# Performance work log

Hardware: AMD Instinct MI355X
Metric: run time of the kernel (lower is better)

The kernel has to match this reference:

```python
import jax, jax.numpy as jnp
import numpy as np
from jax import lax

B, CI, CO, H, W = 8, 128, 256, 56, 56
P, K = 9, 3  # num_paths, kernel_size


def setup_inputs() -> dict:
    key = jax.random.key(0)
    ks = jax.random.split(key, 7)
    s_conv = 1.0 / np.sqrt(CI * K * K)
    s_o1 = 1.0 / np.sqrt(CI)
    s_o2 = 1.0 / np.sqrt(CO // 2)
    return {
        "x": jax.random.normal(ks[0], (B, CI, H, W), dtype=jnp.float32),
        # num_paths independent 3x3 convs, stacked on leading axis
        "kw": jax.random.uniform(ks[1], (P, CO, CI, K, K), jnp.float32, -s_conv, s_conv),
        "kb": jax.random.uniform(ks[2], (P, CO), jnp.float32, -s_conv, s_conv),
        # observer: 1x1 conv CI -> CO//2, tanh, 1x1 conv CO//2 -> P
        "ow1": jax.random.uniform(ks[3], (CO // 2, CI), jnp.float32, -s_o1, s_o1),
        "ob1": jax.random.uniform(ks[4], (CO // 2,), jnp.float32, -s_o1, s_o1),
        "ow2": jax.random.uniform(ks[5], (P, CO // 2), jnp.float32, -s_o2, s_o2),
        "ob2": jax.random.uniform(ks[6], (P,), jnp.float32, -s_o2, s_o2),
    }


def reference(x, kw, kb, ow1, ob1, ow2, ob2):
    p, co, ci, k, _ = kw.shape
    b, _, h, w = x.shape
    # All num_paths convs as a single grouped-output conv: (P*CO, CI, K, K)
    wflat = kw.reshape(p * co, ci, k, k)
    paths = lax.conv_general_dilated(
        x, wflat, window_strides=(1, 1), padding=((1, 1), (1, 1)),
        dimension_numbers=("NCHW", "OIHW", "NCHW"))
    paths = paths + kb.reshape(p * co)[None, :, None, None]
    paths = paths.reshape(b, p, co, h, w)  # [B,P,CO,H,W]

    # observer: two 1x1 convs (pure channel mixes) with tanh in between
    hmid = jnp.tanh(jnp.einsum("bchw,dc->bdhw", x, ow1) + ob1[None, :, None, None])
    scores = jnp.einsum("bdhw,pd->bphw", hmid, ow2) + ob2[None, :, None, None]

    # eval-mode collapse: argmax over paths, pixel-wise hard selection.
    # (one-hot multiply + sum over paths == gather of the winning path)
    idx = jnp.argmax(scores, axis=1)  # [B,H,W]
    out = jnp.take_along_axis(paths, idx[:, None, None, :, :], axis=1)[:, 0]  # [B,CO,H,W]
    return jax.nn.relu(out)  # norm_type='none' -> identity norm
```

## Files before the change

kernel.cpp:

```cpp
#include <hip/hip_runtime.h>
#include <hip/hip_bf16.h>


typedef unsigned int u32;

#define NPIX    25088
#define OFF_LIST 4096
#define OFF_XPAD 907264
#define OFF_W2   7796736
#define OFF_P2R  13105152
#define OFF_OUTC 13205504

__device__ __forceinline__ unsigned short f2bf(float f) {
  u32 u = __builtin_bit_cast(u32, f);
  u32 r = (u + 0x7FFFu + ((u >> 16) & 1u)) >> 16;
  return (unsigned short)r;
}
__device__ __forceinline__ float bflo(u32 w) {
  return __builtin_bit_cast(float, w << 16);
}
__device__ __forceinline__ float bfhi(u32 w) {
  return __builtin_bit_cast(float, w & 0xFFFF0000u);
}

#define GLDS16(g, l)                                                        \
  __builtin_amdgcn_global_load_lds(                                         \
      (const __attribute__((address_space(1))) u32*)(g),                    \
      (__attribute__((address_space(3))) u32*)(l), 16, 0, 0)
#define GLDS4(g, l)                                                         \
  __builtin_amdgcn_global_load_lds(                                         \
      (const __attribute__((address_space(1))) u32*)(g),                    \
      (__attribute__((address_space(3))) u32*)(l), 4, 0, 0)

typedef __attribute__((ext_vector_type(8))) short bf16x8;
typedef __attribute__((ext_vector_type(4))) float f32x4;

__global__ __launch_bounds__(512) void k_front(
    const float* __restrict__ x, const float* __restrict__ kw,
    const float* __restrict__ ow1, const float* __restrict__ ob1,
    const float* __restrict__ ow2, const float* __restrict__ ob2,
    u32* __restrict__ xpad, u32* __restrict__ w2,
    int* __restrict__ cnt, int* __restrict__ list) {
  __shared__ __attribute__((aligned(16))) char smraw[18432];
  __shared__ int lcnt[9], lbase[9];

  int bid = blockIdx.x;
  int tid = threadIdx.x;
  int ln = tid & 63, wv = tid >> 6;

  if (bid < 392) {
    float* xlds = (float*)smraw;
    float* red  = (float*)smraw;
    int dgu = __builtin_amdgcn_readfirstlane(wv);
    int pix0 = bid * 64;
    int b = pix0 / 3136, s0 = pix0 - b * 3136;
    int pix = pix0 + ln;
    const float* xsrc = x + (size_t)b * 401408 + s0 + ln;

    if (tid < 9) lcnt[tid] = 0;

    float h[16];
    const float* o1 = ob1 + dgu * 16;
#pragma unroll
    for (int i = 0; i < 16; ++i) h[i] = o1[i];
    const float* w1b = ow1 + dgu * 16 * 128;

    auto stage = [&](int c, int q) {
      GLDS4(xsrc + (size_t)(8 * c + wv) * 3136, &xlds[q * 512 + wv * 64 + ln]);
    };

    stage(0, 0);
    for (int c = 0; c < 16; ++c) {
      __syncthreads();
      if (c + 1 < 16) stage(c + 1, (c + 1) & 1);
      const float* xq = &xlds[(c & 1) * 512];
      float xc[8];
#pragma unroll
      for (int j = 0; j < 8; ++j) xc[j] = xq[j * 64 + ln];
      int cc = c * 8;
#pragma unroll
      for (int i = 0; i < 16; ++i) {
        const float* wr = w1b + i * 128 + cc;
        float a = h[i];
#pragma unroll
        for (int j = 0; j < 8; ++j) a = fmaf(wr[j], xc[j], a);
        h[i] = a;
      }
    }
    __syncthreads();

#pragma unroll
    for (int i = 0; i < 16; ++i) h[i] = tanhf(h[i]);

#pragma unroll
    for (int p = 0; p < 9; ++p) {
      float sc = 0.f;
      const float* wr = ow2 + p * 128 + dgu * 16;
#pragma unroll
      for (int i = 0; i < 16; ++i) sc = fmaf(wr[i], h[i], sc);
      red[wv * 576 + ln * 9 + p] = sc;
    }
    __syncthreads();

    int bi = 0, slot = 0;
    if (wv == 0) {
      float best = 0.f;
#pragma unroll
      for (int p = 0; p < 9; ++p) {
        float v = ob2[p];
#pragma unroll
        for (int g = 0; g < 8; ++g) v += red[g * 576 + ln * 9 + p];
        if (p == 0 || v > best) { best = v; bi = p; }
      }
      slot = atomicAdd(&lcnt[bi], 1);
    }
    __syncthreads();
    if (tid < 9) lbase[tid] = atomicAdd(&cnt[tid], lcnt[tid]);
    __syncthreads();
    if (wv == 0) list[bi * NPIX + lbase[bi] + slot] = pix;

  } else if (bid < 840) {
    u32* xt = (u32*)smraw;
    int bh = bid - 392;
    int b = bh / 56, hh = bh - b * 56;
    const float* xr = x + (size_t)b * 401408 + hh * 56;
#pragma unroll
    for (int r = 0; r < 8; ++r) {
      int ci = wv * 16 + 2 * r;
      if (ln < 56) {
        float f0 = xr[(size_t)ci * 3136 + ln];
        float f1 = xr[(size_t)(ci + 1) * 3136 + ln];
        xt[ln * 65 + (ci >> 1)] = (u32)f2bf(f0) | ((u32)f2bf(f1) << 16);
      }
    }
    __syncthreads();
    u32* orow = xpad + (size_t)(b * 58 + hh + 1) * 58 * 64;
    for (int w = wv; w < 56; w += 8)
      orow[(w + 1) * 64 + ln] = xt[w * 65 + ln];
    if (wv == 0) orow[ln] = 0;
    else if (wv == 1) orow[57 * 64 + ln] = 0;
    if (hh == 0) {
      u32* hrow = xpad + (size_t)(b * 58) * 58 * 64;
      for (int i = tid; i < 58 * 64; i += 512) hrow[i] = 0;
    } else if (hh == 55) {
      u32* hrow = xpad + (size_t)(b * 58 + 57) * 58 * 64;
      for (int i = tid; i < 58 * 64; i += 512) hrow[i] = 0;
    }

  } else {
    float* kt = (float*)smraw;
    int base = (bid - 840) * 4;
    const float* src = kw + (size_t)base * 1152;
#pragma unroll
    for (int i = 0; i < 9; ++i) kt[i * 512 + tid] = src[i * 512 + tid];
    __syncthreads();
    for (int t = tid; t < 2304; t += 512) {
      int pl = t / 576, d = t - pl * 576;
      int tap = d >> 6, cp = d & 63;
      float v0 = kt[pl * 1152 + 18 * cp + tap];
      float v1 = kt[pl * 1152 + 18 * cp + 9 + tap];
      w2[(size_t)(base + pl) * 576 + d] = (u32)f2bf(v0) | ((u32)f2bf(v1) << 16);
    }
  }
}

__global__ __launch_bounds__(256, 4) void k_conv(
    const int* __restrict__ cnt, const int* __restrict__ list,
    const char* __restrict__ xpadB, const char* __restrict__ w2B,
    const float* __restrict__ kb, unsigned short* __restrict__ outcH,
    int* __restrict__ pix2row) {
  __shared__ short Wlds[2][4096];
  __shared__ short Plds[2][2048];
  __shared__ int offsB[64];
  __shared__ float kbl[128];

  int bid = blockIdx.x;
  int half = bid & 1, tb = bid >> 1;
  int p = -1, cntp = 0, baseP = 0, accb = 0;
  for (int pp = 0; pp < 9; ++pp) {
    int c = cnt[pp];
    int tt = (c + 63) >> 6;
    if (p < 0) {
      if (tb < tt) { p = pp; cntp = c; baseP = accb; }
      else tb -= tt;
    }
    accb += c;
  }
  if (p < 0) return;
  int nbase = tb * 64;
  int tid = threadIdx.x;

  if (tid < 64) {
    int g = nbase + tid;
    bool v = g < cntp;
    int pixid = list[p * NPIX + (v ? g : nbase)];
    int b = pixid / 3136, s = pixid - b * 3136;
    int h = s / 56, w = s - h * 56;
    offsB[tid] = ((b * 58 + h) * 58 + w) * 256;
    if (v && half == 0) pix2row[pixid] = baseP + g;
  }
  if (tid < 128) kbl[tid] = kb[p * 256 + half * 128 + tid];
  __syncthreads();

  int segsw = ((tid & 3) ^ ((tid >> 3) & 3)) * 16;
  int na = tid >> 2;
  int offP = offsB[na] + segsw;
  const char* wrow = w2B + (size_t)(p * 256 + half * 128) * 2304;
  const char* wp0 = wrow + (size_t)na * 2304 + segsw;
  const char* wp1 = wrow + (size_t)(64 + na) * 2304 + segsw;

  auto stage = [&](int c, int q) {
    int tap = c >> 2, kc = c & 3;
    int wko = tap * 256 + kc * 64;
    int tapoff = ((tap / 3) * 58 + (tap % 3)) * 256 + kc * 64;
    GLDS16(wp0 + wko, &Wlds[q][tid * 8]);
    GLDS16(wp1 + wko, &Wlds[q][2048 + tid * 8]);
    GLDS16(xpadB + (size_t)(offP + tapoff), &Plds[q][tid * 8]);
  };

  f32x4 acc[4][2];
#pragma unroll
  for (int mt = 0; mt < 4; ++mt)
#pragma unroll
    for (int nt = 0; nt < 2; ++nt) acc[mt][nt] = (f32x4)0.f;

  int lane = tid & 63, wave = tid >> 6;
  int wm = wave >> 1, wn = wave & 1;
  int l15 = lane & 15, quad = lane >> 4;
  int slot = (quad ^ ((l15 >> 1) & 3)) * 8;
  int mrow = wm * 64 + l15;
  int nrow = wn * 32 + l15;

  stage(0, 0);
  for (int c = 0; c < 36; ++c) {
    __syncthreads();
    if (c + 1 < 36) stage(c + 1, (c + 1) & 1);
    int q = c & 1;
    bf16x8 af[4], bfr[2];
#pragma unroll
    for (int mt = 0; mt < 4; ++mt)
      af[mt] = *(const bf16x8*)&Wlds[q][(mrow + mt * 16) * 32 + slot];
#pragma unroll
    for (int nt = 0; nt < 2; ++nt)
      bfr[nt] = *(const bf16x8*)&Plds[q][(nrow + nt * 16) * 32 + slot];
#pragma unroll
    for (int mt = 0; mt < 4; ++mt)
#pragma unroll
      for (int nt = 0; nt < 2; ++nt)
        acc[mt][nt] = __builtin_amdgcn_mfma_f32_16x16x32_bf16(
            af[mt], bfr[nt], acc[mt][nt], 0, 0, 0);
  }

#pragma unroll
  for (int nt = 0; nt < 2; ++nt) {
    int n = wn * 32 + nt * 16 + l15;
    if ((nbase + n) >= cntp) continue;
    size_t rowb = (size_t)(baseP + nbase + n) * 256 + half * 128;
#pragma unroll
    for (int mt = 0; mt < 4; ++mt) {
      int co0 = wm * 64 + mt * 16 + quad * 4;
      float v0 = acc[mt][nt][0] + kbl[co0 + 0];
      float v1 = acc[mt][nt][1] + kbl[co0 + 1];
      float v2 = acc[mt][nt][2] + kbl[co0 + 2];
      float v3 = acc[mt][nt][3] + kbl[co0 + 3];
      v0 = v0 > 0.f ? v0 : 0.f;  v1 = v1 > 0.f ? v1 : 0.f;
      v2 = v2 > 0.f ? v2 : 0.f;  v3 = v3 > 0.f ? v3 : 0.f;
      u32 lo = (u32)f2bf(v0) | ((u32)f2bf(v1) << 16);
      u32 hi = (u32)f2bf(v2) | ((u32)f2bf(v3) << 16);
      *(u32*)&outcH[rowb + co0]     = lo;
      *(u32*)&outcH[rowb + co0 + 2] = hi;
    }
  }
}

__global__ __launch_bounds__(256) void k_out(
    const int* __restrict__ pix2row, const u32* __restrict__ outcU,
    float* __restrict__ out) {
  int tid = threadIdx.x;
  int pl = tid & 63, coq = tid >> 6;
  int pix = blockIdx.x * 64 + pl;
  int b = pix / 3136, s = pix - b * 3136;
  int row = pix2row[pix];
  const u32* src = outcU + (size_t)row * 128 + coq * 32;
  float* dst = out + (size_t)b * 802816 + s;
#pragma unroll
  for (int j = 0; j < 8; ++j) {
    uint4 w = *(const uint4*)(src + j * 4);
    int co = coq * 64 + j * 8;
    dst[(size_t)(co + 0) * 3136] = bflo(w.x);
    dst[(size_t)(co + 1) * 3136] = bfhi(w.x);
    dst[(size_t)(co + 2) * 3136] = bflo(w.y);
    dst[(size_t)(co + 3) * 3136] = bfhi(w.y);
    dst[(size_t)(co + 4) * 3136] = bflo(w.z);
    dst[(size_t)(co + 5) * 3136] = bfhi(w.z);
    dst[(size_t)(co + 6) * 3136] = bflo(w.w);
    dst[(size_t)(co + 7) * 3136] = bfhi(w.w);
  }
}

extern "C" void kernel_launch(void* const* d_in, const int* in_sizes, int n_in,
                              void* d_out, int out_size, void* d_ws, size_t ws_size,
                              hipStream_t stream) {
  const float* x   = (const float*)d_in[0];
  const float* kw  = (const float*)d_in[1];
  const float* kb  = (const float*)d_in[2];
  const float* ow1 = (const float*)d_in[3];
  const float* ob1 = (const float*)d_in[4];
  const float* ow2 = (const float*)d_in[5];
  const float* ob2 = (const float*)d_in[6];
  float* out = (float*)d_out;
  char* ws = (char*)d_ws;

  int* cnt  = (int*)(ws);
  int* list = (int*)(ws + OFF_LIST);
  u32* xpad = (u32*)(ws + OFF_XPAD);
  u32* w2   = (u32*)(ws + OFF_W2);
  int* p2r  = (int*)(ws + OFF_P2R);
  unsigned short* outc = (unsigned short*)(ws + OFF_OUTC);

  hipMemsetAsync(cnt, 0, 64, stream);

  k_front<<<1416, 512, 0, stream>>>(x, kw, ow1, ob1, ow2, ob2, xpad, w2,
                                    cnt, list);
  k_conv<<<802, 256, 0, stream>>>(cnt, list, (const char*)xpad, (const char*)w2,
                                  kb, outc, p2r);
  k_out<<<392, 256, 0, stream>>>(p2r, (const u32*)outc, out);
}
```

Measured before the change: 164.0 us.

## Scatter conv output by pixel id, drop pix2row indirection, register-prefetch observer input

The conv kernel now writes each output row straight to the row indexed by the pixel id, not to a compacted per-path row. This removes the pix2row map and the dependent indirect load in the output kernel. The output kernel stages 64 contiguous pixel rows through padded LDS before the channel-major writes. The observer stage in k_front replaces its LDS double buffer and barriers with a three-deep register prefetch of x, at the cost of more VGPRs and scattered row writes from the conv kernel.

```diff
diff --git a/kernel.cpp b/kernel.cpp
--- a/kernel.cpp
+++ b/kernel.cpp
@@ -8,8 +8,7 @@
 #define OFF_LIST 4096
 #define OFF_XPAD 907264
 #define OFF_W2   7796736
-#define OFF_P2R  13105152
-#define OFF_OUTC 13205504
+#define OFF_OUTP 13105152
 
 __device__ __forceinline__ unsigned short f2bf(float f) {
   u32 u = __builtin_bit_cast(u32, f);
@@ -27,10 +26,6 @@
   __builtin_amdgcn_global_load_lds(                                         \
       (const __attribute__((address_space(1))) u32*)(g),                    \
       (__attribute__((address_space(3))) u32*)(l), 16, 0, 0)
-#define GLDS4(g, l)                                                         \
-  __builtin_amdgcn_global_load_lds(                                         \
-      (const __attribute__((address_space(1))) u32*)(g),                    \
-      (__attribute__((address_space(3))) u32*)(l), 4, 0, 0)
 
 typedef __attribute__((ext_vector_type(8))) short bf16x8;
 typedef __attribute__((ext_vector_type(4))) float f32x4;
@@ -49,13 +44,11 @@
   int ln = tid & 63, wv = tid >> 6;
 
   if (bid < 392) {
-    float* xlds = (float*)smraw;
-    float* red  = (float*)smraw;
+    float* red = (float*)smraw;
     int dgu = __builtin_amdgcn_readfirstlane(wv);
-    int pix0 = bid * 64;
-    int b = pix0 / 3136, s0 = pix0 - b * 3136;
-    int pix = pix0 + ln;
-    const float* xsrc = x + (size_t)b * 401408 + s0 + ln;
+    int pix = bid * 64 + ln;
+    int b = pix / 3136, s = pix - b * 3136;
+    const float* xb = x + (size_t)b * 401408 + s;
 
     if (tid < 9) lcnt[tid] = 0;
 
@@ -65,29 +58,30 @@
     for (int i = 0; i < 16; ++i) h[i] = o1[i];
     const float* w1b = ow1 + dgu * 16 * 128;
 
-    auto stage = [&](int c, int q) {
-      GLDS4(xsrc + (size_t)(8 * c + wv) * 3136, &xlds[q * 512 + wv * 64 + ln]);
-    };
-
-    stage(0, 0);
+    float bufs[3][8];
+#pragma unroll
+    for (int j = 0; j < 8; ++j) bufs[0][j] = xb[(size_t)j * 3136];
+#pragma unroll
+    for (int j = 0; j < 8; ++j) bufs[1][j] = xb[(size_t)(8 + j) * 3136];
+
+#pragma unroll
     for (int c = 0; c < 16; ++c) {
-      __syncthreads();
-      if (c + 1 < 16) stage(c + 1, (c + 1) & 1);
-      const float* xq = &xlds[(c & 1) * 512];
-      float xc[8];
-#pragma unroll
-      for (int j = 0; j < 8; ++j) xc[j] = xq[j * 64 + ln];
-      int cc = c * 8;
+      if (c + 2 < 16) {
+        const int bi = (c + 2) % 3;
+#pragma unroll
+        for (int j = 0; j < 8; ++j)
+          bufs[bi][j] = xb[(size_t)((c + 2) * 8 + j) * 3136];
+      }
+      const int cur = c % 3;
 #pragma unroll
       for (int i = 0; i < 16; ++i) {
-        const float* wr = w1b + i * 128 + cc;
+        const float* wr = w1b + i * 128 + c * 8;
         float a = h[i];
 #pragma unroll
-        for (int j = 0; j < 8; ++j) a = fmaf(wr[j], xc[j], a);
+        for (int j = 0; j < 8; ++j) a = fmaf(wr[j], bufs[cur][j], a);
         h[i] = a;
       }
     }
-    __syncthreads();
 
 #pragma unroll
     for (int i = 0; i < 16; ++i) h[i] = tanhf(h[i]);
@@ -167,24 +161,22 @@
 __global__ __launch_bounds__(256, 4) void k_conv(
     const int* __restrict__ cnt, const int* __restrict__ list,
     const char* __restrict__ xpadB, const char* __restrict__ w2B,
-    const float* __restrict__ kb, unsigned short* __restrict__ outcH,
-    int* __restrict__ pix2row) {
+    const float* __restrict__ kb, unsigned short* __restrict__ outp) {
   __shared__ short Wlds[2][4096];
   __shared__ short Plds[2][2048];
-  __shared__ int offsB[64];
+  __shared__ int offsB[64], pixSB[64];
   __shared__ float kbl[128];
 
   int bid = blockIdx.x;
   int half = bid & 1, tb = bid >> 1;
-  int p = -1, cntp = 0, baseP = 0, accb = 0;
+  int p = -1, cntp = 0;
   for (int pp = 0; pp < 9; ++pp) {
     int c = cnt[pp];
     int tt = (c + 63) >> 6;
     if (p < 0) {
-      if (tb < tt) { p = pp; cntp = c; baseP = accb; }
+      if (tb < tt) { p = pp; cntp = c; }
       else tb -= tt;
     }
-    accb += c;
   }
   if (p < 0) return;
   int nbase = tb * 64;
@@ -192,12 +184,11 @@
 
   if (tid < 64) {
     int g = nbase + tid;
-    bool v = g < cntp;
-    int pixid = list[p * NPIX + (v ? g : nbase)];
+    int pixid = list[p * NPIX + (g < cntp ? g : nbase)];
     int b = pixid / 3136, s = pixid - b * 3136;
     int h = s / 56, w = s - h * 56;
     offsB[tid] = ((b * 58 + h) * 58 + w) * 256;
-    if (v && half == 0) pix2row[pixid] = baseP + g;
+    pixSB[tid] = pixid;
   }
   if (tid < 128) kbl[tid] = kb[p * 256 + half * 128 + tid];
   __syncthreads();
@@ -255,7 +246,7 @@
   for (int nt = 0; nt < 2; ++nt) {
     int n = wn * 32 + nt * 16 + l15;
     if ((nbase + n) >= cntp) continue;
-    size_t rowb = (size_t)(baseP + nbase + n) * 256 + half * 128;
+    size_t rowb = (size_t)pixSB[n] * 256 + half * 128;
 #pragma unroll
     for (int mt = 0; mt < 4; ++mt) {
       int co0 = wm * 64 + mt * 16 + quad * 4;
@@ -267,34 +258,32 @@
       v2 = v2 > 0.f ? v2 : 0.f;  v3 = v3 > 0.f ? v3 : 0.f;
       u32 lo = (u32)f2bf(v0) | ((u32)f2bf(v1) << 16);
       u32 hi = (u32)f2bf(v2) | ((u32)f2bf(v3) << 16);
-      *(u32*)&outcH[rowb + co0]     = lo;
-      *(u32*)&outcH[rowb + co0 + 2] = hi;
+      *(u32*)&outp[rowb + co0]     = lo;
+      *(u32*)&outp[rowb + co0 + 2] = hi;
     }
   }
 }
 
 __global__ __launch_bounds__(256) void k_out(
-    const int* __restrict__ pix2row, const u32* __restrict__ outcU,
-    float* __restrict__ out) {
+    const u32* __restrict__ outp, float* __restrict__ out) {
+  __shared__ u32 t[64 * 129];
   int tid = threadIdx.x;
-  int pl = tid & 63, coq = tid >> 6;
-  int pix = blockIdx.x * 64 + pl;
-  int b = pix / 3136, s = pix - b * 3136;
-  int row = pix2row[pix];
-  const u32* src = outcU + (size_t)row * 128 + coq * 32;
+  int pix0 = blockIdx.x * 64;
+  const u32* src = outp + (size_t)pix0 * 128;
+  for (int i = tid; i < 8192; i += 256)
+    t[(i >> 7) * 129 + (i & 127)] = src[i];
+  __syncthreads();
+
+  int ln = tid & 63, coq = tid >> 6;
+  int b = pix0 / 3136, s = pix0 - b * 3136 + ln;
   float* dst = out + (size_t)b * 802816 + s;
-#pragma unroll
-  for (int j = 0; j < 8; ++j) {
-    uint4 w = *(const uint4*)(src + j * 4);
-    int co = coq * 64 + j * 8;
-    dst[(size_t)(co + 0) * 3136] = bflo(w.x);
-    dst[(size_t)(co + 1) * 3136] = bfhi(w.x);
-    dst[(size_t)(co + 2) * 3136] = bflo(w.y);
-    dst[(size_t)(co + 3) * 3136] = bfhi(w.y);
-    dst[(size_t)(co + 4) * 3136] = bflo(w.z);
-    dst[(size_t)(co + 5) * 3136] = bfhi(w.z);
-    dst[(size_t)(co + 6) * 3136] = bflo(w.w);
-    dst[(size_t)(co + 7) * 3136] = bfhi(w.w);
+  const u32* row = &t[ln * 129 + coq * 32];
+#pragma unroll
+  for (int j = 0; j < 32; ++j) {
+    u32 w = row[j];
+    int co = 2 * (coq * 32 + j);
+    dst[(size_t)co * 3136]       = bflo(w);
+    dst[(size_t)(co + 1) * 3136] = bfhi(w);
   }
 }
 
@@ -315,14 +304,13 @@
   int* list = (int*)(ws + OFF_LIST);
   u32* xpad = (u32*)(ws + OFF_XPAD);
   u32* w2   = (u32*)(ws + OFF_W2);
-  int* p2r  = (int*)(ws + OFF_P2R);
-  unsigned short* outc = (unsigned short*)(ws + OFF_OUTC);
+  unsigned short* outp = (unsigned short*)(ws + OFF_OUTP);
 
   hipMemsetAsync(cnt, 0, 64, stream);
 
   k_front<<<1416, 512, 0, stream>>>(x, kw, ow1, ob1, ow2, ob2, xpad, w2,
                                     cnt, list);
   k_conv<<<802, 256, 0, stream>>>(cnt, list, (const char*)xpad, (const char*)w2,
-                                  kb, outc, p2r);
-  k_out<<<392, 256, 0, stream>>>(p2r, (const u32*)outc, out);
-}
+                                  kb, outp);
+  k_out<<<392, 256, 0, stream>>>((const u32*)outp, out);
+}
```

After: 192.2 us. +17.3%, slower.
